# Kernel optimization log

Hardware: AMD Instinct MI355X
Metric: run time of the kernel (lower is better)

The kernel has to match this reference:

```python
import jax, jax.numpy as jnp
import numpy as np

EPS = 1e-6
SIGMA_C = 2.0
PAD = 0
VOCAB = 100
D_EMB = 384


def setup_inputs() -> dict:
    key = jax.random.key(0)
    k1, k2, k3 = jax.random.split(key, 3)
    B, L = 32, 1025  # L odd so durs[:,1::2] and durs[:,2::2] align
    text = jax.random.randint(k1, (B, L), 0, VOCAB)
    durs = jax.random.randint(k2, (B, L), 0, 4)
    emb_table = jax.random.normal(k3, (VOCAB, D_EMB), dtype=jnp.float32)
    return {"text": text, "durs": durs, "emb_table": emb_table, "total_time": 2048}


def reference(text, durs, emb_table, total_time):
    # --- merge blank/token pairs (as in GaussianEmbedding.forward) ---
    text_m = jnp.concatenate([text[:, :1], text[:, 1::2]], axis=1)              # [B,N]
    durs_m = jnp.concatenate([durs[:, :1], durs[:, 1::2] + durs[:, 2::2]], axis=1)  # [B,N]
    embed = emb_table[text_m]                                                    # [B,N,E]

    # --- Gaussian length regulation ---
    d = durs_m.astype(jnp.float32)
    cum = jnp.cumsum(d, axis=-1)                 # [B,N] end times
    c = cum - 0.5 * d                            # [B,N] token centers
    sig = d / SIGMA_C + EPS                      # [B,N]
    t = jnp.arange(total_time, dtype=jnp.float32) + 0.5  # [T] frame midpoints

    # Normal pdf weights [B,T,N]
    z = (t[None, :, None] - c[:, None, :]) / sig[:, None, :]
    w = jnp.exp(-0.5 * z * z) / (sig[:, None, :] * jnp.sqrt(2.0 * jnp.pi))
    # zero weight for pad tokens, normalize over tokens
    w = jnp.where((text_m == PAD)[:, None, :], 0.0, w)
    w = w / (w.sum(-1, keepdims=True) + EPS)
    # zero frames beyond each sample's total duration
    valid = t[None, :] < cum[:, -1:]             # [B,T]
    w = jnp.where(valid[..., None], w, 0.0)

    return jnp.einsum('btn,bne->bte', w, embed)  # [B,T,E]
```

## Files before the change

### kernel.cpp

```cpp
#include <hip/hip_runtime.h>
#include <hip/hip_bf16.h>

#define BATCH 32
#define LSEQ 1025
#define TT 2048
#define NTOK 513
#define EMB 384
#define FT 32
#define WMAX 120
#define INV_SQRT_2PI 0.3989422804014327f

__device__ inline float* scan513(float* src, float* dst) {
  for (int off = 1; off < NTOK; off <<= 1) {
    for (int i = threadIdx.x; i < NTOK; i += 256) {
      float v = src[i];
      if (i >= off) v += src[i - off];
      dst[i] = v;
    }
    __syncthreads();
    float* t = src; src = dst; dst = t;
  }
  return src;
}

__global__ __launch_bounds__(256) void prep_kernel(
    const int* __restrict__ text, const int* __restrict__ durs,
    float2* __restrict__ kept, int* __restrict__ counts,
    float* __restrict__ totals) {
  const int b = blockIdx.x;
  const int tid = threadIdx.x;
  __shared__ float s_a[NTOK], s_b[NTOK];
  __shared__ float s_c[NTOK];
  __shared__ float s_d[NTOK];
  __shared__ int s_tok[NTOK];

  const int* tb = text + b * LSEQ;
  const int* db = durs + b * LSEQ;
  for (int n = tid; n < NTOK; n += 256) {
    int dm, tk;
    if (n == 0) { dm = db[0]; tk = tb[0]; }
    else { dm = db[2 * n - 1] + db[2 * n]; tk = tb[2 * n - 1]; }
    s_d[n] = (float)dm;
    s_a[n] = (float)dm;
    s_tok[n] = tk;
  }
  __syncthreads();
  float* cum = scan513(s_a, s_b);
  for (int n = tid; n < NTOK; n += 256) {
    s_c[n] = cum[n] - 0.5f * s_d[n];
  }
  if (tid == 0) totals[b] = cum[NTOK - 1];
  __syncthreads();
  float* flagbuf = (cum == s_a) ? s_a : s_b;
  float* other = (cum == s_a) ? s_b : s_a;
  for (int n = tid; n < NTOK; n += 256) {
    flagbuf[n] = (s_d[n] >= 1.0f && s_tok[n] != 0) ? 1.0f : 0.0f;
  }
  __syncthreads();
  float* incl = scan513(flagbuf, other);
  for (int n = tid; n < NTOK; n += 256) {
    float d = s_d[n];
    int tk = s_tok[n];
    if (d >= 1.0f && tk != 0) {
      int pos = (int)incl[n] - 1;
      int packed = ((int)d << 17) | (tk * EMB);
      kept[b * NTOK + pos] = make_float2(s_c[n], __int_as_float(packed));
    }
  }
  if (tid == 0) counts[b] = (int)incl[NTOK - 1];
}

__global__ __launch_bounds__(384) void frames_kernel(
    const float2* __restrict__ kept, const int* __restrict__ counts,
    const float* __restrict__ totals, const float* __restrict__ emb,
    float* __restrict__ out) {
  const int t0 = blockIdx.x * FT;
  const int b = blockIdx.y;
  const int tid = threadIdx.x;

  __shared__ float4 s_tk[WMAX];
  __shared__ float s_reach[WMAX];
  __shared__ float s_w[WMAX * FT];
  __shared__ float s_factor[FT];

  const int M = counts[b];
  const float total = totals[b];
  const float2* kb = kept + b * NTOK;

  const float loB = (float)t0 - 40.5f;
  const float hiB = (float)t0 + 71.5f;
  int l = 0, r = M;
  while (l < r) { int m = (l + r) >> 1; if (kb[m].x < loB) l = m + 1; else r = m; }
  const int lo = l;
  r = M;
  while (l < r) { int m = (l + r) >> 1; if (kb[m].x <= hiB) l = m + 1; else r = m; }
  int win = l - lo;
  if (win > WMAX) win = WMAX;
  if ((float)t0 + 0.5f >= total) win = 0;

  for (int i = tid; i < win; i += 384) {
    float2 kv = kb[lo + i];
    int packed = __float_as_int(kv.y);
    int d = packed >> 17;
    int off = packed & 0x1FFFF;
    float df = (float)d;
    float inv_sig = 1.0f / (0.5f * df + 1e-6f);
    s_tk[i] = make_float4(kv.x, inv_sig, INV_SQRT_2PI * inv_sig,
                          __int_as_float(off));
    s_reach[i] = 6.7f * df + 1e-4f;
  }
  __syncthreads();

  const float t0f = (float)t0 + 0.5f;
  const int pairs = win * FT;
  for (int idx = tid; idx < pairs; idx += 384) {
    const int n = idx >> 5, f = idx & (FT - 1);
    const float4 tk = s_tk[n];
    const float z = (t0f + (float)f - tk.x) * tk.y;
    s_w[idx] = tk.z * __expf(-0.5f * z * z);
  }
  __syncthreads();

  if (tid < FT) {
    float s = 0.f;
    for (int n = 0; n < win; ++n) s += s_w[n * FT + tid];
    const float tf = t0f + (float)tid;
    s_factor[tid] = (tf < total) ? 1.0f / (s + 1e-6f) : 0.0f;
  }
  __syncthreads();

  const int fh = tid / 192;
  const int c2 = (tid % 192) * 2;
  const int fbase = fh * 16;
  float2 acc[16];
#pragma unroll
  for (int k = 0; k < 16; ++k) acc[k] = make_float2(0.f, 0.f);

  const float fLo = (float)(t0 + fbase) + 0.5f;
  const float fHi = fLo + 15.0f;
  for (int n = 0; n < win; ++n) {
    const float4 tk = s_tk[n];
    const float reach = s_reach[n];
    if (tk.x + reach < fLo || tk.x - reach > fHi) continue;
    const float2 v = *(const float2*)(emb + (__float_as_int(tk.w) & 0x1FFFF)
                                      + c2);
    const float4* wp = (const float4*)(s_w + n * FT + fbase);
#pragma unroll
    for (int q = 0; q < 4; ++q) {
      const float4 w4 = wp[q];
      float2& a0 = acc[4 * q + 0];
      a0.x += w4.x * v.x; a0.y += w4.x * v.y;
      float2& a1 = acc[4 * q + 1];
      a1.x += w4.y * v.x; a1.y += w4.y * v.y;
      float2& a2 = acc[4 * q + 2];
      a2.x += w4.z * v.x; a2.y += w4.z * v.y;
      float2& a3 = acc[4 * q + 3];
      a3.x += w4.w * v.x; a3.y += w4.w * v.y;
    }
  }

  float* obase = out + ((size_t)b * TT + t0 + fbase) * EMB + c2;
#pragma unroll
  for (int k = 0; k < 16; ++k) {
    const float fac = s_factor[fbase + k];
    *(float2*)(obase + (size_t)k * EMB) =
        make_float2(acc[k].x * fac, acc[k].y * fac);
  }
}

extern "C" void kernel_launch(void* const* d_in, const int* in_sizes, int n_in,
                              void* d_out, int out_size, void* d_ws,
                              size_t ws_size, hipStream_t stream) {
  const int* text = (const int*)d_in[0];
  const int* durs = (const int*)d_in[1];
  const float* emb = (const float*)d_in[2];
  float* out = (float*)d_out;

  float2* kept = (float2*)d_ws;
  int* counts = (int*)(kept + BATCH * NTOK);
  float* totals = (float*)(counts + BATCH);

  prep_kernel<<<BATCH, 256, 0, stream>>>(text, durs, kept, counts, totals);
  frames_kernel<<<dim3(TT / FT, BATCH), 384, 0, stream>>>(kept, counts, totals,
                                                          emb, out);
}
```

Measured before the change: 135.3 us.

## Compact touching tokens via ballot and chunk window with float4 thread mapping

The frames kernel now walks the token window in chunks of 64. In each chunk a wave ballot compacts only the tokens whose Gaussian reach overlaps the 32-frame tile, instead of a fixed window capped at 120 with a per-warp skip test. Thread mapping changes to 4 groups of 8 frames by 96 float4 channel lanes, so embedding loads are wider and each thread holds 32 accumulators. Normalisation sums are kept in shared memory across chunks, and the factor is computed at store time. The risk is extra synchronisation per chunk and higher register pressure.

```diff
diff --git a/kernel.cpp b/kernel.cpp
--- a/kernel.cpp
+++ b/kernel.cpp
@@ -7,7 +7,7 @@
 #define NTOK 513
 #define EMB 384
 #define FT 32
-#define WMAX 120
+#define WMAX 64
 #define INV_SQRT_2PI 0.3989422804014327f
 
 __device__ inline float* scan513(float* src, float* dst) {
@@ -77,94 +77,118 @@
   const int t0 = blockIdx.x * FT;
   const int b = blockIdx.y;
   const int tid = threadIdx.x;
+  const int g = tid / 96;
+  const int q = tid % 96;
+  const int fbase = g * 8;
 
   __shared__ float4 s_tk[WMAX];
-  __shared__ float s_reach[WMAX];
-  __shared__ float s_w[WMAX * FT];
-  __shared__ float s_factor[FT];
+  __shared__ float s_w[WMAX][FT];
+  __shared__ float s_sum[FT];
+  __shared__ int s_cnt;
 
   const int M = counts[b];
   const float total = totals[b];
   const float2* kb = kept + b * NTOK;
 
-  const float loB = (float)t0 - 40.5f;
-  const float hiB = (float)t0 + 71.5f;
-  int l = 0, r = M;
-  while (l < r) { int m = (l + r) >> 1; if (kb[m].x < loB) l = m + 1; else r = m; }
-  const int lo = l;
-  r = M;
-  while (l < r) { int m = (l + r) >> 1; if (kb[m].x <= hiB) l = m + 1; else r = m; }
-  int win = l - lo;
-  if (win > WMAX) win = WMAX;
-  if ((float)t0 + 0.5f >= total) win = 0;
-
-  for (int i = tid; i < win; i += 384) {
-    float2 kv = kb[lo + i];
-    int packed = __float_as_int(kv.y);
-    int d = packed >> 17;
-    int off = packed & 0x1FFFF;
-    float df = (float)d;
-    float inv_sig = 1.0f / (0.5f * df + 1e-6f);
-    s_tk[i] = make_float4(kv.x, inv_sig, INV_SQRT_2PI * inv_sig,
-                          __int_as_float(off));
-    s_reach[i] = 6.7f * df + 1e-4f;
-  }
-  __syncthreads();
+  const float tileLo = (float)t0 + 0.5f;
+  const float tileHi = (float)t0 + 31.5f;
+  const bool tile_valid = tileLo < total;
+
+  int lo = 0, hi = 0;
+  if (tile_valid) {
+    const float loB = (float)t0 - 40.5f;
+    const float hiB = (float)t0 + 72.5f;
+    int l = 0, r = M;
+    while (l < r) { int m = (l + r) >> 1; if (kb[m].x < loB) l = m + 1; else r = m; }
+    lo = l;
+    r = M;
+    while (l < r) { int m = (l + r) >> 1; if (kb[m].x <= hiB) l = m + 1; else r = m; }
+    hi = l;
+  }
+
+  if (tid < FT) s_sum[tid] = 0.f;
+
+  float4 acc[8];
+#pragma unroll
+  for (int k = 0; k < 8; ++k) acc[k] = make_float4(0.f, 0.f, 0.f, 0.f);
 
   const float t0f = (float)t0 + 0.5f;
-  const int pairs = win * FT;
-  for (int idx = tid; idx < pairs; idx += 384) {
-    const int n = idx >> 5, f = idx & (FT - 1);
-    const float4 tk = s_tk[n];
-    const float z = (t0f + (float)f - tk.x) * tk.y;
-    s_w[idx] = tk.z * __expf(-0.5f * z * z);
-  }
-  __syncthreads();
-
-  if (tid < FT) {
-    float s = 0.f;
-    for (int n = 0; n < win; ++n) s += s_w[n * FT + tid];
-    const float tf = t0f + (float)tid;
-    s_factor[tid] = (tf < total) ? 1.0f / (s + 1e-6f) : 0.0f;
-  }
-  __syncthreads();
-
-  const int fh = tid / 192;
-  const int c2 = (tid % 192) * 2;
-  const int fbase = fh * 16;
-  float2 acc[16];
+
+  for (int pos = lo; pos < hi; pos += WMAX) {
+    const int cand = min(hi - pos, WMAX);
+    __syncthreads();
+    if (tid < 64) {
+      bool touch = false;
+      float cc = 0.f, df = 0.f;
+      int packed = 0;
+      if (tid < cand) {
+        float2 kv = kb[pos + tid];
+        cc = kv.x;
+        packed = __float_as_int(kv.y);
+        df = (float)(packed >> 17);
+        const float reach = 6.7f * df + 1e-4f;
+        touch = (cc + reach >= tileLo) && (cc - reach <= tileHi);
+      }
+      const unsigned long long mask = __ballot(touch);
+      if (touch) {
+        const int slot = __popcll(mask & ((1ull << (tid & 63)) - 1));
+        const float inv_sig = 1.0f / (0.5f * df + 1e-6f);
+        s_tk[slot] = make_float4(cc, inv_sig, INV_SQRT_2PI * inv_sig,
+                                 __int_as_float(packed & 0x1FFFF));
+      }
+      if (tid == 0) s_cnt = __popcll(mask);
+    }
+    __syncthreads();
+    const int cnt = s_cnt;
+
+    const int pairs = cnt * FT;
+    for (int idx = tid; idx < pairs; idx += 384) {
+      const int n = idx >> 5, f = idx & (FT - 1);
+      const float4 tk = s_tk[n];
+      const float z = (t0f + (float)f - tk.x) * tk.y;
+      s_w[n][f] = tk.z * __expf(-0.5f * z * z);
+    }
+    __syncthreads();
+
+    if (tid < FT) {
+      float s = 0.f;
+      for (int n = 0; n < cnt; ++n) s += s_w[n][tid];
+      s_sum[tid] += s;
+    }
+
+    for (int n = 0; n < cnt; ++n) {
+      const float4 tk = s_tk[n];
+      const float4 v = *(const float4*)(emb + __float_as_int(tk.w) + q * 4);
+      const float4 w0 = *(const float4*)&s_w[n][fbase];
+      const float4 w1 = *(const float4*)&s_w[n][fbase + 4];
+      acc[0].x += w0.x * v.x; acc[0].y += w0.x * v.y;
+      acc[0].z += w0.x * v.z; acc[0].w += w0.x * v.w;
+      acc[1].x += w0.y * v.x; acc[1].y += w0.y * v.y;
+      acc[1].z += w0.y * v.z; acc[1].w += w0.y * v.w;
+      acc[2].x += w0.z * v.x; acc[2].y += w0.z * v.y;
+      acc[2].z += w0.z * v.z; acc[2].w += w0.z * v.w;
+      acc[3].x += w0.w * v.x; acc[3].y += w0.w * v.y;
+      acc[3].z += w0.w * v.z; acc[3].w += w0.w * v.w;
+      acc[4].x += w1.x * v.x; acc[4].y += w1.x * v.y;
+      acc[4].z += w1.x * v.z; acc[4].w += w1.x * v.w;
+      acc[5].x += w1.y * v.x; acc[5].y += w1.y * v.y;
+      acc[5].z += w1.y * v.z; acc[5].w += w1.y * v.w;
+      acc[6].x += w1.z * v.x; acc[6].y += w1.z * v.y;
+      acc[6].z += w1.z * v.z; acc[6].w += w1.z * v.w;
+      acc[7].x += w1.w * v.x; acc[7].y += w1.w * v.y;
+      acc[7].z += w1.w * v.z; acc[7].w += w1.w * v.w;
+    }
+  }
+  __syncthreads();
+
+  float* obase = out + ((size_t)b * TT + t0 + fbase) * EMB + q * 4;
 #pragma unroll
-  for (int k = 0; k < 16; ++k) acc[k] = make_float2(0.f, 0.f);
-
-  const float fLo = (float)(t0 + fbase) + 0.5f;
-  const float fHi = fLo + 15.0f;
-  for (int n = 0; n < win; ++n) {
-    const float4 tk = s_tk[n];
-    const float reach = s_reach[n];
-    if (tk.x + reach < fLo || tk.x - reach > fHi) continue;
-    const float2 v = *(const float2*)(emb + (__float_as_int(tk.w) & 0x1FFFF)
-                                      + c2);
-    const float4* wp = (const float4*)(s_w + n * FT + fbase);
-#pragma unroll
-    for (int q = 0; q < 4; ++q) {
-      const float4 w4 = wp[q];
-      float2& a0 = acc[4 * q + 0];
-      a0.x += w4.x * v.x; a0.y += w4.x * v.y;
-      float2& a1 = acc[4 * q + 1];
-      a1.x += w4.y * v.x; a1.y += w4.y * v.y;
-      float2& a2 = acc[4 * q + 2];
-      a2.x += w4.z * v.x; a2.y += w4.z * v.y;
-      float2& a3 = acc[4 * q + 3];
-      a3.x += w4.w * v.x; a3.y += w4.w * v.y;
-    }
-  }
-
-  float* obase = out + ((size_t)b * TT + t0 + fbase) * EMB + c2;
-#pragma unroll
-  for (int k = 0; k < 16; ++k) {
-    const float fac = s_factor[fbase + k];
-    *(float2*)(obase + (size_t)k * EMB) =
-        make_float2(acc[k].x * fac, acc[k].y * fac);
+  for (int k = 0; k < 8; ++k) {
+    const float tf = t0f + (float)(fbase + k);
+    const float fac = (tf < total) ? 1.0f / (s_sum[fbase + k] + 1e-6f) : 0.0f;
+    *(float4*)(obase + (size_t)k * EMB) =
+        make_float4(acc[k].x * fac, acc[k].y * fac,
+                    acc[k].z * fac, acc[k].w * fac);
   }
 }
 
```

Measured after the change: 139.1 us. +2.8%, slower.
